# Kernel optimization log

Measured on AMD Instinct MI355X. Metric: run time of the kernel, lower is better.

Reference implementation:

```python
import jax, jax.numpy as jnp
import numpy as np

B, K, T, V, H = 32, 5, 20, 9488, 1024


def setup_inputs() -> dict:
    key = jax.random.key(0)
    k0, k1, k2, k3, k4 = jax.random.split(key, 5)
    logprobs = jax.nn.log_softmax(jax.random.normal(k0, (B * K, V), jnp.float32), -1)
    beam_seq = jax.random.randint(k1, (B, K, T), 0, V)
    beam_seq_logprobs = jax.random.normal(k2, (B, K, T, V), jnp.float32)
    beam_logprobs_sum = jax.random.normal(k3, (B, K), jnp.float32)
    state = jax.random.normal(k4, (2, B * K, H), jnp.float32)
    return {"logprobs": logprobs, "beam_seq": beam_seq,
            "beam_seq_logprobs": beam_seq_logprobs,
            "beam_logprobs_sum": beam_logprobs_sum, "state": state,
            "beam_size": K, "t": T}


def reference(logprobs, beam_seq, beam_seq_logprobs, beam_logprobs_sum, state, beam_size, t):
    # One beam_step of CaptionModel.beam_search.
    batch = beam_logprobs_sum.shape[0]
    vocab = logprobs.shape[-1]
    lp = logprobs.reshape(batch, -1, vocab)                  # [B, K, V]
    cand = beam_logprobs_sum[:, :, None] + lp                # [B, K, V]
    flat = cand.reshape(batch, -1)                           # [B, K*V]
    # torch.sort(desc)[:, :beam_size] == top_k (sorted descending)
    ys, ix = jax.lax.top_k(flat, beam_size)                  # [B, K]
    beam_ix = ix // vocab                                    # source beam  [B, K]
    selected_ix = ix % vocab                                 # chosen word  [B, K]
    brange = jnp.arange(batch)[:, None]
    state_ix = (beam_ix + brange * lp.shape[1]).reshape(-1)  # [B*K]

    if t > 0:
        beam_seq = beam_seq[brange, beam_ix]                             # [B, K, t]
        beam_seq_logprobs = beam_seq_logprobs[brange, beam_ix]           # [B, K, t, V]
    beam_seq = jnp.concatenate([beam_seq, selected_ix[:, :, None].astype(beam_seq.dtype)], -1)

    beam_logprobs_sum = (jnp.take_along_axis(beam_logprobs_sum, beam_ix, 1)
                         + jnp.take_along_axis(lp.reshape(batch, -1), ix, 1))  # [B, K]

    beam_lp = lp[brange, beam_ix]                            # [B, K, V]
    beam_seq_logprobs = jnp.concatenate([beam_seq_logprobs, beam_lp[:, :, None, :]], 2)

    new_state = state[:, state_ix]                           # [layers, B*K, H]
    return beam_seq, beam_seq_logprobs, beam_logprobs_sum, new_state
```

## Files before the change

### kernel.cpp

```cpp
#include <hip/hip_runtime.h>

#define BB 32
#define KK 5
#define TT 20
#define VV 9488
#define HH 1024
#define NSPLIT 16
#define CHUNK (VV / NSPLIT)

#define OFF1 3360
#define OFF2 31883040
#define OFF3 31883200

#define N1F4 7969920
#define NSF4 81920
#define TOTF4 (N1F4 + NSF4)

typedef float f4 __attribute__((ext_vector_type(4)));
typedef unsigned long long u64;

__device__ __forceinline__ bool better(float av, int ai, float bv, int bi) {
    return (av > bv) || (av == bv && ai < bi);
}

__global__ __launch_bounds__(256) void topk_part_kernel(
    const float* __restrict__ logprobs,
    const float* __restrict__ sums,
    float* __restrict__ pv,
    int*   __restrict__ pi)
{
    const int b    = blockIdx.x / NSPLIT;
    const int part = blockIdx.x % NSPLIT;
    const int tid  = threadIdx.x;
    const int v0   = part * CHUNK;

    float tv[5]; int ti[5];
#pragma unroll
    for (int j = 0; j < 5; ++j) { tv[j] = -INFINITY; ti[j] = 0x7FFFFF00 + j; }

    for (int k = 0; k < KK; ++k) {
        const float s = sums[b * KK + k];
        const float* lp = logprobs + (size_t)(b * KK + k) * VV;
        for (int v = v0 + tid; v < v0 + CHUNK; v += 256) {
            const float val = s + lp[v];
            const int idx = k * VV + v;
            if (better(val, idx, tv[4], ti[4])) {
                int pos = 4;
#pragma unroll
                for (int j = 3; j >= 0; --j)
                    if (better(val, idx, tv[j], ti[j])) pos = j;
#pragma unroll
                for (int j = 4; j > 0; --j) {
                    if (j > pos) { tv[j] = tv[j-1]; ti[j] = ti[j-1]; }
                }
                tv[pos] = val; ti[pos] = idx;
            }
        }
    }

    __shared__ float sv[256 * 5];
    __shared__ int   si[256 * 5];

    for (int stride = 128; stride >= 1; stride >>= 1) {
        if (tid >= stride && tid < 2 * stride) {
#pragma unroll
            for (int j = 0; j < 5; ++j) { sv[tid*5+j] = tv[j]; si[tid*5+j] = ti[j]; }
        }
        __syncthreads();
        if (tid < stride) {
            float bv[5]; int bi[5];
#pragma unroll
            for (int j = 0; j < 5; ++j) { bv[j] = sv[(tid+stride)*5+j]; bi[j] = si[(tid+stride)*5+j]; }
            float ov[5]; int oi[5];
            int ia = 0, ib = 0;
#pragma unroll
            for (int n = 0; n < 5; ++n) {
                if (better(tv[ia], ti[ia], bv[ib], bi[ib])) { ov[n] = tv[ia]; oi[n] = ti[ia]; ++ia; }
                else                                        { ov[n] = bv[ib]; oi[n] = bi[ib]; ++ib; }
            }
#pragma unroll
            for (int j = 0; j < 5; ++j) { tv[j] = ov[j]; ti[j] = oi[j]; }
        }
        __syncthreads();
    }

    if (tid == 0) {
#pragma unroll
        for (int j = 0; j < 5; ++j) {
            pv[(size_t)blockIdx.x * 5 + j] = tv[j];
            pi[(size_t)blockIdx.x * 5 + j] = ti[j];
        }
    }
}

__device__ __forceinline__ void merge_sorted5(float av[5], int ai[5],
                                              const float bv[5], const int bi[5]) {
    float ov[5]; int oi[5];
#pragma unroll
    for (int n = 0; n < 5; ++n) {
        float mv = 0.f; int mi = 0;
#pragma unroll
        for (int i = 0; i <= n; ++i) {
            const int j = n - i;
            float cv; int ci;
            if (better(av[i], ai[i], bv[j], bi[j])) { cv = av[i]; ci = ai[i]; }
            else                                    { cv = bv[j]; ci = bi[j]; }
            if (i == 0 || better(mv, mi, cv, ci)) { mv = cv; mi = ci; }
        }
        ov[n] = mv; oi[n] = mi;
    }
#pragma unroll
    for (int n = 0; n < 5; ++n) { av[n] = ov[n]; ai[n] = oi[n]; }
}

__global__ __launch_bounds__(64) void merge_kernel(
    const float* __restrict__ pv,
    const int*   __restrict__ pi,
    const float* __restrict__ logprobs,
    const int*   __restrict__ beam_seq_in,
    const float* __restrict__ bslp_in,
    const float* __restrict__ state_in,
    u64* __restrict__ srcrow,
    u64* __restrict__ srcst,
    float* __restrict__ out)
{
    const int b   = blockIdx.x;
    const int tid = threadIdx.x;

    float tv[5]; int ti[5];
    if (tid < NSPLIT) {
        const size_t base = ((size_t)b * NSPLIT + tid) * 5;
#pragma unroll
        for (int j = 0; j < 5; ++j) { tv[j] = pv[base + j]; ti[j] = pi[base + j]; }
    } else {
#pragma unroll
        for (int j = 0; j < 5; ++j) { tv[j] = -INFINITY; ti[j] = 0x7FFFFF00 + j; }
    }

#pragma unroll
    for (int st = 1; st <= 8; st <<= 1) {
        float bv[5]; int bi[5];
#pragma unroll
        for (int j = 0; j < 5; ++j) {
            bv[j] = __shfl_xor(tv[j], st);
            bi[j] = __shfl_xor(ti[j], st);
        }
        merge_sorted5(tv, ti, bv, bi);
    }
#pragma unroll
    for (int j = 0; j < 5; ++j) {
        tv[j] = __shfl(tv[j], 0);
        ti[j] = __shfl(ti[j], 0);
    }
    int beam[5], sel[5];
#pragma unroll
    for (int j = 0; j < 5; ++j) { beam[j] = ti[j] / VV; sel[j] = ti[j] - beam[j] * VV; }

    for (int rr = tid; rr < KK * (TT + 1); rr += 64) {
        const int k = rr / (TT + 1), t = rr % (TT + 1);
        int bm = 0, sl = 0;
#pragma unroll
        for (int j = 0; j < 5; ++j) if (k == j) { bm = beam[j]; sl = sel[j]; }
        const float* src = (t < TT)
            ? bslp_in  + ((size_t)((b * KK + bm) * TT + t)) * VV
            : logprobs + (size_t)(b * KK + bm) * VV;
        srcrow[b * KK * (TT + 1) + rr] = (u64)(uintptr_t)src;
        const int val = (t < TT) ? beam_seq_in[(size_t)(b * KK + bm) * TT + t] : sl;
        out[(size_t)b * KK * (TT + 1) + rr] = (float)val;
    }

    if (tid < 10) {
        const int s = tid / 5, k = tid % 5;
        int bm = 0;
#pragma unroll
        for (int j = 0; j < 5; ++j) if (k == j) bm = beam[j];
        srcst[s * (BB * KK) + b * KK + k] =
            (u64)(uintptr_t)(state_in + ((size_t)s * (BB * KK) + b * KK + bm) * HH);
    }

    if (tid == 0) {
#pragma unroll
        for (int j = 0; j < 5; ++j) out[OFF2 + b * KK + j] = tv[j];
    }
}

__global__ __launch_bounds__(256) void copy_kernel(
    const u64* __restrict__ srcrow,
    const u64* __restrict__ srcst,
    float* __restrict__ out)
{
    f4* __restrict__ dst1 = (f4*)(out + OFF1);
    f4* __restrict__ dst3 = (f4*)(out + OFF3);
    const int stride = gridDim.x * 256;
    for (int idx = blockIdx.x * 256 + threadIdx.x; idx < TOTF4; idx += stride) {
        if (idx < N1F4) {
            const unsigned row = (unsigned)idx / 2372u;
            const unsigned col = (unsigned)idx - row * 2372u;
            const f4* __restrict__ s = (const f4*)(uintptr_t)srcrow[row];
            f4 v = s[col];
            __builtin_nontemporal_store(v, &dst1[idx]);
        } else {
            const int j = idx - N1F4;
            const int r = j >> 8, col = j & 255;
            const f4* __restrict__ s = (const f4*)(uintptr_t)srcst[r];
            f4 v = s[col];
            __builtin_nontemporal_store(v, &dst3[j]);
        }
    }
}

extern "C" void kernel_launch(void* const* d_in, const int* in_sizes, int n_in,
                              void* d_out, int out_size, void* d_ws, size_t ws_size,
                              hipStream_t stream) {
    const float* logprobs = (const float*)d_in[0];
    const int*   beam_seq = (const int*)  d_in[1];
    const float* bslp     = (const float*)d_in[2];
    const float* sums     = (const float*)d_in[3];
    const float* state    = (const float*)d_in[4];

    u64*   srcrow = (u64*)d_ws;
    u64*   srcst  = srcrow + BB * KK * (TT + 1);
    float* pv     = (float*)(srcst + 2 * BB * KK);
    int*   pi     = (int*)(pv + BB * NSPLIT * 5);
    float* out    = (float*)d_out;

    topk_part_kernel<<<BB * NSPLIT, 256, 0, stream>>>(logprobs, sums, pv, pi);
    merge_kernel<<<BB, 64, 0, stream>>>(pv, pi, logprobs, beam_seq, bslp, state,
                                        srcrow, srcst, out);
    copy_kernel<<<2048, 256, 0, stream>>>(srcrow, srcst, out);
}
```

Baseline: 58.55 us.

## Fuse top-k merge into partial kernel via last-block atomic counter

Removes the separate merge kernel launch. Each partial top-k block publishes its result and increments a per-batch atomic counter, and the last block to finish does the final merge, the index gathers and the pointer-table writes. This saves one kernel launch and its dependency gap, but adds a memset launch to reset the counters plus threadfence and atomic overhead.

New measurement: 125.8 us. 115% more time.

```diff
diff --git a/kernel.cpp b/kernel.cpp
--- a/kernel.cpp
+++ b/kernel.cpp
@@ -23,11 +23,38 @@
     return (av > bv) || (av == bv && ai < bi);
 }
 
+__device__ __forceinline__ void merge_sorted5(float av[5], int ai[5],
+                                              const float bv[5], const int bi[5]) {
+    float ov[5]; int oi[5];
+#pragma unroll
+    for (int n = 0; n < 5; ++n) {
+        float mv = 0.f; int mi = 0;
+#pragma unroll
+        for (int i = 0; i <= n; ++i) {
+            const int j = n - i;
+            float cv; int ci;
+            if (better(av[i], ai[i], bv[j], bi[j])) { cv = av[i]; ci = ai[i]; }
+            else                                    { cv = bv[j]; ci = bi[j]; }
+            if (i == 0 || better(mv, mi, cv, ci)) { mv = cv; mi = ci; }
+        }
+        ov[n] = mv; oi[n] = mi;
+    }
+#pragma unroll
+    for (int n = 0; n < 5; ++n) { av[n] = ov[n]; ai[n] = oi[n]; }
+}
+
 __global__ __launch_bounds__(256) void topk_part_kernel(
     const float* __restrict__ logprobs,
     const float* __restrict__ sums,
+    const int*   __restrict__ beam_seq_in,
+    const float* __restrict__ bslp_in,
+    const float* __restrict__ state_in,
+    int*   __restrict__ counters,
     float* __restrict__ pv,
-    int*   __restrict__ pi)
+    int*   __restrict__ pi,
+    u64*   __restrict__ srcrow,
+    u64*   __restrict__ srcst,
+    float* __restrict__ out)
 {
     const int b    = blockIdx.x / NSPLIT;
     const int part = blockIdx.x % NSPLIT;
@@ -84,103 +111,80 @@
         __syncthreads();
     }
 
+    __shared__ int do_merge;
     if (tid == 0) {
 #pragma unroll
         for (int j = 0; j < 5; ++j) {
             pv[(size_t)blockIdx.x * 5 + j] = tv[j];
             pi[(size_t)blockIdx.x * 5 + j] = ti[j];
         }
-    }
-}
-
-__device__ __forceinline__ void merge_sorted5(float av[5], int ai[5],
-                                              const float bv[5], const int bi[5]) {
-    float ov[5]; int oi[5];
-#pragma unroll
-    for (int n = 0; n < 5; ++n) {
-        float mv = 0.f; int mi = 0;
-#pragma unroll
-        for (int i = 0; i <= n; ++i) {
-            const int j = n - i;
-            float cv; int ci;
-            if (better(av[i], ai[i], bv[j], bi[j])) { cv = av[i]; ci = ai[i]; }
-            else                                    { cv = bv[j]; ci = bi[j]; }
-            if (i == 0 || better(mv, mi, cv, ci)) { mv = cv; mi = ci; }
-        }
-        ov[n] = mv; oi[n] = mi;
-    }
-#pragma unroll
-    for (int n = 0; n < 5; ++n) { av[n] = ov[n]; ai[n] = oi[n]; }
-}
-
-__global__ __launch_bounds__(64) void merge_kernel(
-    const float* __restrict__ pv,
-    const int*   __restrict__ pi,
-    const float* __restrict__ logprobs,
-    const int*   __restrict__ beam_seq_in,
-    const float* __restrict__ bslp_in,
-    const float* __restrict__ state_in,
-    u64* __restrict__ srcrow,
-    u64* __restrict__ srcst,
-    float* __restrict__ out)
-{
-    const int b   = blockIdx.x;
-    const int tid = threadIdx.x;
-
-    float tv[5]; int ti[5];
-    if (tid < NSPLIT) {
-        const size_t base = ((size_t)b * NSPLIT + tid) * 5;
-#pragma unroll
-        for (int j = 0; j < 5; ++j) { tv[j] = pv[base + j]; ti[j] = pi[base + j]; }
-    } else {
-#pragma unroll
-        for (int j = 0; j < 5; ++j) { tv[j] = -INFINITY; ti[j] = 0x7FFFFF00 + j; }
-    }
-
-#pragma unroll
-    for (int st = 1; st <= 8; st <<= 1) {
-        float bv[5]; int bi[5];
-#pragma unroll
-        for (int j = 0; j < 5; ++j) {
-            bv[j] = __shfl_xor(tv[j], st);
-            bi[j] = __shfl_xor(ti[j], st);
-        }
-        merge_sorted5(tv, ti, bv, bi);
-    }
+        __threadfence();
+        do_merge = (atomicAdd(&counters[b], 1) == NSPLIT - 1);
+    }
+    __syncthreads();
+    if (!do_merge) return;
+
+    __threadfence();
+
+    if (tid < 64) {
+        if (tid < NSPLIT) {
+            const size_t base = ((size_t)b * NSPLIT + tid) * 5;
+#pragma unroll
+            for (int j = 0; j < 5; ++j) { tv[j] = pv[base + j]; ti[j] = pi[base + j]; }
+        } else {
+#pragma unroll
+            for (int j = 0; j < 5; ++j) { tv[j] = -INFINITY; ti[j] = 0x7FFFFF00 + j; }
+        }
+#pragma unroll
+        for (int st = 1; st <= 8; st <<= 1) {
+            float bv[5]; int bi[5];
+#pragma unroll
+            for (int j = 0; j < 5; ++j) {
+                bv[j] = __shfl_xor(tv[j], st);
+                bi[j] = __shfl_xor(ti[j], st);
+            }
+            merge_sorted5(tv, ti, bv, bi);
+        }
+        if (tid == 0) {
+#pragma unroll
+            for (int j = 0; j < 5; ++j) { sv[j] = tv[j]; si[j] = ti[j]; }
+        }
+    }
+    __syncthreads();
+
+    float ftv[5]; int beam[5], sel[5];
 #pragma unroll
     for (int j = 0; j < 5; ++j) {
-        tv[j] = __shfl(tv[j], 0);
-        ti[j] = __shfl(ti[j], 0);
-    }
-    int beam[5], sel[5];
-#pragma unroll
-    for (int j = 0; j < 5; ++j) { beam[j] = ti[j] / VV; sel[j] = ti[j] - beam[j] * VV; }
-
-    for (int rr = tid; rr < KK * (TT + 1); rr += 64) {
-        const int k = rr / (TT + 1), t = rr % (TT + 1);
+        ftv[j] = sv[j];
+        const int idx = si[j];
+        beam[j] = idx / VV;
+        sel[j]  = idx - beam[j] * VV;
+    }
+
+    if (tid < KK * (TT + 1)) {
+        const int k = tid / (TT + 1), t = tid % (TT + 1);
         int bm = 0, sl = 0;
 #pragma unroll
         for (int j = 0; j < 5; ++j) if (k == j) { bm = beam[j]; sl = sel[j]; }
         const float* src = (t < TT)
             ? bslp_in  + ((size_t)((b * KK + bm) * TT + t)) * VV
             : logprobs + (size_t)(b * KK + bm) * VV;
-        srcrow[b * KK * (TT + 1) + rr] = (u64)(uintptr_t)src;
+        srcrow[b * KK * (TT + 1) + tid] = (u64)(uintptr_t)src;
         const int val = (t < TT) ? beam_seq_in[(size_t)(b * KK + bm) * TT + t] : sl;
-        out[(size_t)b * KK * (TT + 1) + rr] = (float)val;
-    }
-
-    if (tid < 10) {
-        const int s = tid / 5, k = tid % 5;
+        out[(size_t)b * KK * (TT + 1) + tid] = (float)val;
+    }
+    else if (tid >= 128 && tid < 138) {
+        const int r = tid - 128;
+        const int s = r / 5, k = r % 5;
         int bm = 0;
 #pragma unroll
         for (int j = 0; j < 5; ++j) if (k == j) bm = beam[j];
         srcst[s * (BB * KK) + b * KK + k] =
             (u64)(uintptr_t)(state_in + ((size_t)s * (BB * KK) + b * KK + bm) * HH);
     }
-
-    if (tid == 0) {
-#pragma unroll
-        for (int j = 0; j < 5; ++j) out[OFF2 + b * KK + j] = tv[j];
+    else if (tid >= 192 && tid < 197) {
+        const int j = tid - 192;
+        out[OFF2 + b * KK + j] = ftv[j];
     }
 }
 
@@ -218,14 +222,18 @@
     const float* sums     = (const float*)d_in[3];
     const float* state    = (const float*)d_in[4];
 
-    u64*   srcrow = (u64*)d_ws;
-    u64*   srcst  = srcrow + BB * KK * (TT + 1);
-    float* pv     = (float*)(srcst + 2 * BB * KK);
-    int*   pi     = (int*)(pv + BB * NSPLIT * 5);
-    float* out    = (float*)d_out;
-
-    topk_part_kernel<<<BB * NSPLIT, 256, 0, stream>>>(logprobs, sums, pv, pi);
-    merge_kernel<<<BB, 64, 0, stream>>>(pv, pi, logprobs, beam_seq, bslp, state,
-                                        srcrow, srcst, out);
+    int*   counters = (int*)d_ws;
+    u64*   srcrow   = (u64*)((char*)d_ws + 128);
+    u64*   srcst    = srcrow + BB * KK * (TT + 1);
+    float* pv       = (float*)(srcst + 2 * BB * KK);
+    int*   pi       = (int*)(pv + BB * NSPLIT * 5);
+    float* out      = (float*)d_out;
+
+    hipMemsetAsync(counters, 0, 128, stream);
+
+    topk_part_kernel<<<BB * NSPLIT, 256, 0, stream>>>(
+        logprobs, sums, beam_seq, bslp, state,
+        counters, pv, pi, srcrow, srcst, out);
+
     copy_kernel<<<2048, 256, 0, stream>>>(srcrow, srcst, out);
 }
```
